# Performance work log

Measured on AMD Instinct MI355X. Metric: run time of the kernel, lower is better.

Reference implementation:

```python
import jax, jax.numpy as jnp
import numpy as np

N_NODES = 50000
N_EDGES = 1600000
D_IN = 128
D_HID = 128
D_OUT = 128


def setup_inputs() -> dict:
    key = jax.random.key(0)
    k1, k2, k3, k4, k5, k6 = jax.random.split(key, 6)
    x = jax.random.normal(k1, (N_NODES, D_IN), dtype=jnp.float32)
    edge_index = jax.random.randint(k2, (2, N_EDGES), 0, N_NODES, dtype=jnp.int64)
    # glorot-ish init for GCNConv linear weights; bias zeros-like but randomized small
    W1 = jax.random.normal(k3, (D_IN, D_HID), dtype=jnp.float32) * (1.0 / np.sqrt(D_IN))
    b1 = jax.random.normal(k4, (D_HID,), dtype=jnp.float32) * 0.01
    W2 = jax.random.normal(k5, (D_HID, D_OUT), dtype=jnp.float32) * (1.0 / np.sqrt(D_HID))
    b2 = jax.random.normal(k6, (D_OUT,), dtype=jnp.float32) * 0.01
    return {"x": x, "edge_index": edge_index, "W1": W1, "b1": b1, "W2": W2, "b2": b2}


def gcn_conv(x, src, dst, W, b, n_nodes):
    # PyG GCNConv: add self-loops, symmetric normalization deg^-1/2, lin -> aggregate -> +bias
    loop = jnp.arange(n_nodes, dtype=src.dtype)
    s = jnp.concatenate([src, loop])  # [E+N]
    d = jnp.concatenate([dst, loop])  # [E+N]
    deg = jax.ops.segment_sum(jnp.ones_like(d, dtype=x.dtype), d, num_segments=n_nodes)
    dinv = jnp.where(deg > 0, jax.lax.rsqrt(deg), 0.0)
    norm = dinv[s] * dinv[d]  # [E+N]
    h = x @ W  # [N, F_out]
    msg = h[s] * norm[:, None]  # gather + scale: [E+N, F_out]
    out = jax.ops.segment_sum(msg, d, num_segments=n_nodes)  # scatter-add
    return out + b


def reference(x, edge_index, W1, b1, W2, b2):
    src, dst = edge_index[0], edge_index[1]
    h = gcn_conv(x, src, dst, W1, b1, N_NODES)
    h = jnp.where(h >= 0, h, 0.1 * h)  # LeakyReLU(0.1)
    h = gcn_conv(h, src, dst, W2, b2, N_NODES)
    return h.mean(axis=1)  # [N]
```

## Files before the change

kernel.cpp:

```cpp
#include <hip/hip_runtime.h>
#include <hip/hip_bf16.h>


#define N_NODES 50000
#define NPAD 50048
#define D 128
#define BK 196
#define CHUNK 4096

typedef unsigned int uint;
typedef unsigned short u16;
typedef __attribute__((ext_vector_type(8))) short short8;
typedef __attribute__((ext_vector_type(4))) float floatx4;

__device__ __forceinline__ u16 cvt_bf16(float f) {
    uint u = __float_as_uint(f);
    return (u16)((u + 0x7fffu + ((u >> 16) & 1u)) >> 16);
}
__device__ __forceinline__ uint pack_bf2(float a, float b) {
    return (uint)cvt_bf16(a) | ((uint)cvt_bf16(b) << 16);
}

__global__ void hist_w2m_kernel(const int* __restrict__ dst, uint* __restrict__ H,
                                const float* __restrict__ W2, const float* __restrict__ b2,
                                float* __restrict__ w2m, uint* __restrict__ counter,
                                int E, int CHN) {
    int t = threadIdx.x, c = blockIdx.x;
    if (c < CHN) {
        __shared__ uint h[BK];
        if (t < BK) h[t] = 0;
        __syncthreads();
        int e0 = c * CHUNK;
        for (int i = t; i < CHUNK; i += 256) {
            int e = e0 + i;
            if (e < E) atomicAdd(&h[dst[e] >> 8], 1u);
        }
        __syncthreads();
        if (t < BK) H[t * CHN + c] = h[t];
    } else {
        if (t < 128) {
            float s = 0.f;
            for (int j = 0; j < 128; j++) s += W2[t * 128 + j];
            w2m[t] = s * (1.0f / 128.0f);
        } else if (t == 128) {
            float s = 0.f;
            for (int j = 0; j < 128; j++) s += b2[j];
            w2m[128] = s * (1.0f / 128.0f);
        } else if (t == 129) {
            *counter = 0;
        }
    }
}

__global__ void scan_kernel(uint* __restrict__ H, uint* __restrict__ T, uint* __restrict__ B,
                            int* __restrict__ row, uint* __restrict__ counter,
                            int CHN, int E, int N) {
    __shared__ uint s[256];
    __shared__ uint ticket_sh;
    int t = threadIdx.x, b = blockIdx.x;
    uint carry = 0;
    for (int base = 0; base < CHN; base += 256) {
        int idx = base + t;
        uint v = (idx < CHN) ? H[b * CHN + idx] : 0u;
        s[t] = v;
        __syncthreads();
#pragma unroll
        for (int off = 1; off < 256; off <<= 1) {
            uint u = (t >= off) ? s[t - off] : 0u;
            __syncthreads();
            s[t] += u;
            __syncthreads();
        }
        if (idx < CHN) H[b * CHN + idx] = carry + s[t] - v;
        carry += s[255];
        __syncthreads();
    }
    if (t == 0) {
        atomicExch(&T[b], carry);
        __threadfence();
        ticket_sh = atomicAdd(counter, 1);
    }
    __syncthreads();
    if (ticket_sh == (uint)(gridDim.x - 1)) {
        __threadfence();
        uint v = (t < BK) ? atomicAdd(&T[t], 0u) : 0u;
        s[t] = v;
        __syncthreads();
#pragma unroll
        for (int off = 1; off < 256; off <<= 1) {
            uint u = (t >= off) ? s[t - off] : 0u;
            __syncthreads();
            s[t] += u;
            __syncthreads();
        }
        if (t < BK) B[t] = s[t] - v;
        if (t == 0) { B[BK] = (uint)E; row[N] = E; }
    }
}

__global__ void scatter_kernel(const int* __restrict__ src, const int* __restrict__ dst,
                               const uint* __restrict__ H, const uint* __restrict__ B,
                               uint* __restrict__ EB, int E, int CHN) {
    __shared__ uint cur[BK];
    int t = threadIdx.x, c = blockIdx.x;
    if (t < BK) cur[t] = B[t] + H[t * CHN + c];
    __syncthreads();
    int e0 = c * CHUNK;
    for (int i = t; i < CHUNK; i += 256) {
        int e = e0 + i;
        if (e < E) {
            int d = dst[e];
            uint slot = atomicAdd(&cur[d >> 8], 1u);
            EB[slot] = ((uint)(d & 255) << 16) | (uint)src[e];
        }
    }
}

#define WT_STRIDE 136
union SortGemmSmem {
    struct { uint cnt[256], s[256], cur[256]; } sort;
    u16 wt[128 * WT_STRIDE];
};
__global__ __launch_bounds__(256) void sortgemm_kernel(
    const uint* __restrict__ EB, const uint* __restrict__ B,
    int* __restrict__ row, float* __restrict__ dinv, u16* __restrict__ esrc,
    const float* __restrict__ A, const float* __restrict__ W,
    uint* __restrict__ G32, int N, int M) {
    __shared__ SortGemmSmem sm;
    int t = threadIdx.x;

    if (blockIdx.x < BK) {
        int b = blockIdx.x;
        uint base = B[b], ne = B[b + 1] - base;
        sm.sort.cnt[t] = 0;
        __syncthreads();
        for (uint i = t; i < ne; i += 256) atomicAdd(&sm.sort.cnt[EB[base + i] >> 16], 1u);
        __syncthreads();
        uint c = sm.sort.cnt[t];
        sm.sort.s[t] = c;
        __syncthreads();
#pragma unroll
        for (int off = 1; off < 256; off <<= 1) {
            uint u = (t >= off) ? sm.sort.s[t - off] : 0u;
            __syncthreads();
            sm.sort.s[t] += u;
            __syncthreads();
        }
        uint p = sm.sort.s[t] - c;
        int v = (b << 8) + t;
        if (v < N) {
            row[v] = (int)(base + p);
            dinv[v] = rsqrtf((float)(c + 1u));
        }
        sm.sort.cur[t] = base + p;
        __syncthreads();
        for (uint i = t; i < ne; i += 256) {
            uint u = EB[base + i];
            uint slot = atomicAdd(&sm.sort.cur[u >> 16], 1u);
            esrc[slot] = (u16)(u & 0xffffu);
        }
    } else {
        int bid = blockIdx.x - BK;
        for (int i = t; i < 128 * 128; i += 256) {
            int k = i >> 7, n = i & 127;
            sm.wt[n * WT_STRIDE + k] = cvt_bf16(W[i]);
        }
        __syncthreads();

        int wave = t >> 6, lane = t & 63;
        int m = lane & 15, quad = lane >> 4;
        int rowa = bid * 64 + wave * 16 + m;
        int rowc = rowa < M ? rowa : M - 1;
        const float* Arow = A + (long)rowc * D;

        short8 afrag[4];
#pragma unroll
        for (int kt = 0; kt < 4; kt++) {
            int k0 = kt * 32 + quad * 8;
            float4 f0 = *(const float4*)(Arow + k0);
            float4 f1 = *(const float4*)(Arow + k0 + 4);
            short8 af;
            af[0] = (short)cvt_bf16(f0.x); af[1] = (short)cvt_bf16(f0.y);
            af[2] = (short)cvt_bf16(f0.z); af[3] = (short)cvt_bf16(f0.w);
            af[4] = (short)cvt_bf16(f1.x); af[5] = (short)cvt_bf16(f1.y);
            af[6] = (short)cvt_bf16(f1.z); af[7] = (short)cvt_bf16(f1.w);
            afrag[kt] = af;
        }

        int orow0 = bid * 64 + wave * 16;
        for (int n0 = 0; n0 < 128; n0 += 16) {
            floatx4 acc = {0.f, 0.f, 0.f, 0.f};
#pragma unroll
            for (int kt = 0; kt < 4; kt++) {
                short8 bf = *(const short8*)(sm.wt + (n0 + m) * WT_STRIDE + kt * 32 + quad * 8);
                acc = __builtin_amdgcn_mfma_f32_16x16x32_bf16(afrag[kt], bf, acc, 0, 0, 0);
            }
#pragma unroll
            for (int r = 0; r < 4; r++) {
                float val = acc[r];
                float oth = __shfl_xor(val, 1, 64);
                int orow = orow0 + quad * 4 + r;
                if (orow < M && (m & 1) == 0)
                    G32[(long)orow * 64 + ((n0 + m) >> 1)] = pack_bf2(val, oth);
            }
        }
    }
}

__global__ __launch_bounds__(256) void gather_node_kernel(
    const int* __restrict__ row, const u16* __restrict__ esrc,
    const uint* __restrict__ g16, const float* __restrict__ dinv,
    const float* __restrict__ b1, const float* __restrict__ w2m,
    float* __restrict__ mg, int N) {
    int wave = threadIdx.x >> 6;
    int lane = threadIdx.x & 63;
    int sub = lane & 7;
    int nb = lane >> 3;
    int v = blockIdx.x * 4 + wave;
    if (v >= N) return;

    const uint4* gv = (const uint4*)g16;
    float dvv = dinv[v];
    float acc[16];
#pragma unroll
    for (int i = 0; i < 16; i++) acc[i] = 0.f;

#define ACC8(ua, ub, wgt) {                                              \
    uint uu[8] = {(ua).x, (ua).y, (ua).z, (ua).w, (ub).x, (ub).y, (ub).z, (ub).w}; \
    _Pragma("unroll")                                                    \
    for (int i = 0; i < 8; i++) {                                        \
        acc[2*i]   += (wgt) * __uint_as_float(uu[i] << 16);              \
        acc[2*i+1] += (wgt) * __uint_as_float(uu[i] & 0xffff0000u);      \
    } }

    if (nb == 0) {
        long rb = (long)v * 16 + 2 * sub;
        uint4 ua = gv[rb], ub = gv[rb + 1];
        ACC8(ua, ub, dvv)
    }
    int jb = row[v], je = row[v + 1];
    int j = jb + nb;
    if (j < je) {
        int s0 = esrc[j];
        float wA = dinv[s0];
        long r0 = (long)s0 * 16 + 2 * sub;
        uint4 p0 = gv[r0], p1 = gv[r0 + 1];
        j += 8;
        while (j < je) {
            int s1 = esrc[j];
            float wB = dinv[s1];
            long r1 = (long)s1 * 16 + 2 * sub;
            uint4 q0 = gv[r1], q1 = gv[r1 + 1];
            j += 8;
            ACC8(p0, p1, wA)
            p0 = q0; p1 = q1; wA = wB;
        }
        ACC8(p0, p1, wA)
    }
#undef ACC8

#pragma unroll
    for (int i = 0; i < 16; i++) {
        acc[i] += __shfl_xor(acc[i], 8, 64);
        acc[i] += __shfl_xor(acc[i], 16, 64);
        acc[i] += __shfl_xor(acc[i], 32, 64);
    }

    if (nb == 0) {
        const float4* bp = (const float4*)b1;
        const float4* wp = (const float4*)w2m;
        float s = 0.f;
#pragma unroll
        for (int q4 = 0; q4 < 4; q4++) {
            float4 bb = bp[sub * 4 + q4];
            float4 wm = wp[sub * 4 + q4];
            float t0 = dvv * acc[4*q4 + 0] + bb.x; t0 = t0 >= 0.f ? t0 : 0.1f * t0;
            float t1 = dvv * acc[4*q4 + 1] + bb.y; t1 = t1 >= 0.f ? t1 : 0.1f * t1;
            float t2 = dvv * acc[4*q4 + 2] + bb.z; t2 = t2 >= 0.f ? t2 : 0.1f * t2;
            float t3 = dvv * acc[4*q4 + 3] + bb.w; t3 = t3 >= 0.f ? t3 : 0.1f * t3;
            s += t0 * wm.x + t1 * wm.y + t2 * wm.z + t3 * wm.w;
        }
        s += __shfl_xor(s, 1, 64);
        s += __shfl_xor(s, 2, 64);
        s += __shfl_xor(s, 4, 64);
        if (sub == 0) mg[v] = dvv * s;
    }
}

__global__ void out_kernel(const int* __restrict__ row, const u16* __restrict__ esrc,
                           const float* __restrict__ mg, const float* __restrict__ dinv,
                           const float* __restrict__ w2m, float* __restrict__ out, int N) {
    int v = blockIdx.x * blockDim.x + threadIdx.x;
    if (v >= N) return;
    float acc = mg[v];
    int jb = row[v], je = row[v + 1];
    int j = jb;
    for (; j + 8 <= je; j += 8) {
        acc += mg[esrc[j]] + mg[esrc[j + 1]] + mg[esrc[j + 2]] + mg[esrc[j + 3]] +
               mg[esrc[j + 4]] + mg[esrc[j + 5]] + mg[esrc[j + 6]] + mg[esrc[j + 7]];
    }
    for (; j < je; j++) acc += mg[esrc[j]];
    out[v] = dinv[v] * acc + w2m[128];
}

extern "C" void kernel_launch(void* const* d_in, const int* in_sizes, int n_in,
                              void* d_out, int out_size, void* d_ws, size_t ws_size,
                              hipStream_t stream) {
    const float* x  = (const float*)d_in[0];
    const int* ei   = (const int*)d_in[1];
    const float* W1 = (const float*)d_in[2];
    const float* b1 = (const float*)d_in[3];
    const float* W2 = (const float*)d_in[4];
    const float* b2 = (const float*)d_in[5];
    float* out = (float*)d_out;

    const int N = N_NODES;
    const int E = in_sizes[1] / 2;
    const int* src = ei;
    const int* dst = ei + E;
    const int CHN = (E + CHUNK - 1) / CHUNK;
    const int nblocks = (N + 255) / 256;

    float*    dinv    = (float*)d_ws;
    int*      row     = (int*)(dinv + NPAD);
    uint*     B       = (uint*)(row + NPAD + 16);
    float*    w2m     = (float*)(B + 256);
    float*    mg      = w2m + 256;
    uint*     T       = (uint*)(mg + NPAD);
    uint*     counter = T + 256;
    uint*     g16u    = counter + 16;
    u16*      esrc    = (u16*)(g16u + (long)NPAD * 64);
    uint*     H       = (uint*)(esrc + E);
    uint*     EB      = H + BK * CHN;

    hist_w2m_kernel<<<CHN + 1, 256, 0, stream>>>(dst, H, W2, b2, w2m, counter, E, CHN);
    scan_kernel<<<BK, 256, 0, stream>>>(H, T, B, row, counter, CHN, E, N);
    scatter_kernel<<<CHN, 256, 0, stream>>>(src, dst, H, B, EB, E, CHN);
    sortgemm_kernel<<<BK + (N + 63) / 64, 256, 0, stream>>>(EB, B, row, dinv, esrc,
                                                            x, W1, g16u, N, N);
    gather_node_kernel<<<(N + 3) / 4, 256, 0, stream>>>(row, esrc, g16u, dinv, b1, w2m, mg, N);
    out_kernel<<<nblocks, 256, 0, stream>>>(row, esrc, mg, dinv, w2m, out, N);
}
```

Before: 197.8 us.

## Fuse bucket scan into histogram via global atomics; double GEMM rows per block

Removes the separate scan kernel and the per-chunk histogram matrix. Each chunk now atomically adds its bucket counts to global totals, and the last block (chosen by ticket) computes the exclusive bucket offsets. The scatter kernel re-counts its own chunk locally and reserves space with one global atomic per bucket, so bucket placement across chunks becomes nondeterministic. The GEMM part also processes 128 rows per block instead of 64, which halves how often the weights are staged into shared memory but also halves the number of GEMM blocks. A memset is added to clear the counters.

Measured after the change: 209.3 us. 1.06x slower.

```diff
diff --git a/kernel.cpp b/kernel.cpp
--- a/kernel.cpp
+++ b/kernel.cpp
@@ -21,13 +21,17 @@
     return (uint)cvt_bf16(a) | ((uint)cvt_bf16(b) << 16);
 }
 
-__global__ void hist_w2m_kernel(const int* __restrict__ dst, uint* __restrict__ H,
+__global__ void hist_w2m_kernel(const int* __restrict__ dst,
                                 const float* __restrict__ W2, const float* __restrict__ b2,
-                                float* __restrict__ w2m, uint* __restrict__ counter,
-                                int E, int CHN) {
+                                float* __restrict__ w2m,
+                                uint* __restrict__ Tg, uint* __restrict__ counter,
+                                uint* __restrict__ B, uint* __restrict__ cur196,
+                                int* __restrict__ row, int E, int CHN, int N) {
     int t = threadIdx.x, c = blockIdx.x;
     if (c < CHN) {
         __shared__ uint h[BK];
+        __shared__ uint s[256];
+        __shared__ uint ticket_sh;
         if (t < BK) h[t] = 0;
         __syncthreads();
         int e0 = c * CHUNK;
@@ -36,81 +40,68 @@
             if (e < E) atomicAdd(&h[dst[e] >> 8], 1u);
         }
         __syncthreads();
-        if (t < BK) H[t * CHN + c] = h[t];
+        if (t < BK && h[t]) atomicAdd(&Tg[t], h[t]);
+        __syncthreads();
+        if (t == 0) {
+            __threadfence();
+            ticket_sh = atomicAdd(counter, 1);
+        }
+        __syncthreads();
+        if (ticket_sh == (uint)(CHN - 1)) {
+            __threadfence();
+            uint v = (t < BK) ? atomicAdd(&Tg[t], 0u) : 0u;
+            s[t] = v;
+            __syncthreads();
+#pragma unroll
+            for (int off = 1; off < 256; off <<= 1) {
+                uint u = (t >= off) ? s[t - off] : 0u;
+                __syncthreads();
+                s[t] += u;
+                __syncthreads();
+            }
+            if (t < BK) {
+                uint excl = s[t] - v;
+                B[t] = excl;
+                cur196[t] = excl;
+            }
+            if (t == 0) { B[BK] = (uint)E; row[N] = E; }
+        }
     } else {
         if (t < 128) {
-            float s = 0.f;
-            for (int j = 0; j < 128; j++) s += W2[t * 128 + j];
-            w2m[t] = s * (1.0f / 128.0f);
+            float sum = 0.f;
+            for (int j = 0; j < 128; j++) sum += W2[t * 128 + j];
+            w2m[t] = sum * (1.0f / 128.0f);
         } else if (t == 128) {
-            float s = 0.f;
-            for (int j = 0; j < 128; j++) s += b2[j];
-            w2m[128] = s * (1.0f / 128.0f);
-        } else if (t == 129) {
-            *counter = 0;
-        }
-    }
-}
-
-__global__ void scan_kernel(uint* __restrict__ H, uint* __restrict__ T, uint* __restrict__ B,
-                            int* __restrict__ row, uint* __restrict__ counter,
-                            int CHN, int E, int N) {
-    __shared__ uint s[256];
-    __shared__ uint ticket_sh;
-    int t = threadIdx.x, b = blockIdx.x;
-    uint carry = 0;
-    for (int base = 0; base < CHN; base += 256) {
-        int idx = base + t;
-        uint v = (idx < CHN) ? H[b * CHN + idx] : 0u;
-        s[t] = v;
-        __syncthreads();
-#pragma unroll
-        for (int off = 1; off < 256; off <<= 1) {
-            uint u = (t >= off) ? s[t - off] : 0u;
-            __syncthreads();
-            s[t] += u;
-            __syncthreads();
-        }
-        if (idx < CHN) H[b * CHN + idx] = carry + s[t] - v;
-        carry += s[255];
-        __syncthreads();
-    }
-    if (t == 0) {
-        atomicExch(&T[b], carry);
-        __threadfence();
-        ticket_sh = atomicAdd(counter, 1);
-    }
-    __syncthreads();
-    if (ticket_sh == (uint)(gridDim.x - 1)) {
-        __threadfence();
-        uint v = (t < BK) ? atomicAdd(&T[t], 0u) : 0u;
-        s[t] = v;
-        __syncthreads();
-#pragma unroll
-        for (int off = 1; off < 256; off <<= 1) {
-            uint u = (t >= off) ? s[t - off] : 0u;
-            __syncthreads();
-            s[t] += u;
-            __syncthreads();
-        }
-        if (t < BK) B[t] = s[t] - v;
-        if (t == 0) { B[BK] = (uint)E; row[N] = E; }
+            float sum = 0.f;
+            for (int j = 0; j < 128; j++) sum += b2[j];
+            w2m[128] = sum * (1.0f / 128.0f);
+        }
     }
 }
 
 __global__ void scatter_kernel(const int* __restrict__ src, const int* __restrict__ dst,
-                               const uint* __restrict__ H, const uint* __restrict__ B,
-                               uint* __restrict__ EB, int E, int CHN) {
-    __shared__ uint cur[BK];
+                               uint* __restrict__ cur196, uint* __restrict__ EB,
+                               int E, int CHN) {
+    __shared__ uint cnt[BK];
     int t = threadIdx.x, c = blockIdx.x;
-    if (t < BK) cur[t] = B[t] + H[t * CHN + c];
+    if (t < BK) cnt[t] = 0;
     __syncthreads();
     int e0 = c * CHUNK;
     for (int i = t; i < CHUNK; i += 256) {
         int e = e0 + i;
+        if (e < E) atomicAdd(&cnt[dst[e] >> 8], 1u);
+    }
+    __syncthreads();
+    if (t < BK) {
+        uint n = cnt[t];
+        cnt[t] = n ? atomicAdd(&cur196[t], n) : 0u;
+    }
+    __syncthreads();
+    for (int i = t; i < CHUNK; i += 256) {
+        int e = e0 + i;
         if (e < E) {
             int d = dst[e];
-            uint slot = atomicAdd(&cur[d >> 8], 1u);
+            uint slot = atomicAdd(&cnt[d >> 8], 1u);
             EB[slot] = ((uint)(d & 255) << 16) | (uint)src[e];
         }
     }
@@ -169,39 +160,43 @@
 
         int wave = t >> 6, lane = t & 63;
         int m = lane & 15, quad = lane >> 4;
-        int rowa = bid * 64 + wave * 16 + m;
-        int rowc = rowa < M ? rowa : M - 1;
-        const float* Arow = A + (long)rowc * D;
-
-        short8 afrag[4];
-#pragma unroll
-        for (int kt = 0; kt < 4; kt++) {
-            int k0 = kt * 32 + quad * 8;
-            float4 f0 = *(const float4*)(Arow + k0);
-            float4 f1 = *(const float4*)(Arow + k0 + 4);
-            short8 af;
-            af[0] = (short)cvt_bf16(f0.x); af[1] = (short)cvt_bf16(f0.y);
-            af[2] = (short)cvt_bf16(f0.z); af[3] = (short)cvt_bf16(f0.w);
-            af[4] = (short)cvt_bf16(f1.x); af[5] = (short)cvt_bf16(f1.y);
-            af[6] = (short)cvt_bf16(f1.z); af[7] = (short)cvt_bf16(f1.w);
-            afrag[kt] = af;
-        }
-
-        int orow0 = bid * 64 + wave * 16;
-        for (int n0 = 0; n0 < 128; n0 += 16) {
-            floatx4 acc = {0.f, 0.f, 0.f, 0.f};
+
+#pragma unroll
+        for (int rg = 0; rg < 2; rg++) {
+            int rowa = bid * 128 + rg * 64 + wave * 16 + m;
+            int rowc = rowa < M ? rowa : M - 1;
+            const float* Arow = A + (long)rowc * D;
+
+            short8 afrag[4];
 #pragma unroll
             for (int kt = 0; kt < 4; kt++) {
-                short8 bf = *(const short8*)(sm.wt + (n0 + m) * WT_STRIDE + kt * 32 + quad * 8);
-                acc = __builtin_amdgcn_mfma_f32_16x16x32_bf16(afrag[kt], bf, acc, 0, 0, 0);
+                int k0 = kt * 32 + quad * 8;
+                float4 f0 = *(const float4*)(Arow + k0);
+                float4 f1 = *(const float4*)(Arow + k0 + 4);
+                short8 af;
+                af[0] = (short)cvt_bf16(f0.x); af[1] = (short)cvt_bf16(f0.y);
+                af[2] = (short)cvt_bf16(f0.z); af[3] = (short)cvt_bf16(f0.w);
+                af[4] = (short)cvt_bf16(f1.x); af[5] = (short)cvt_bf16(f1.y);
+                af[6] = (short)cvt_bf16(f1.z); af[7] = (short)cvt_bf16(f1.w);
+                afrag[kt] = af;
             }
-#pragma unroll
-            for (int r = 0; r < 4; r++) {
-                float val = acc[r];
-                float oth = __shfl_xor(val, 1, 64);
-                int orow = orow0 + quad * 4 + r;
-                if (orow < M && (m & 1) == 0)
-                    G32[(long)orow * 64 + ((n0 + m) >> 1)] = pack_bf2(val, oth);
+
+            int orow0 = bid * 128 + rg * 64 + wave * 16;
+            for (int n0 = 0; n0 < 128; n0 += 16) {
+                floatx4 acc = {0.f, 0.f, 0.f, 0.f};
+#pragma unroll
+                for (int kt = 0; kt < 4; kt++) {
+                    short8 bf = *(const short8*)(sm.wt + (n0 + m) * WT_STRIDE + kt * 32 + quad * 8);
+                    acc = __builtin_amdgcn_mfma_f32_16x16x32_bf16(afrag[kt], bf, acc, 0, 0, 0);
+                }
+#pragma unroll
+                for (int r = 0; r < 4; r++) {
+                    float val = acc[r];
+                    float oth = __shfl_xor(val, 1, 64);
+                    int orow = orow0 + quad * 4 + r;
+                    if (orow < M && (m & 1) == 0)
+                        G32[(long)orow * 64 + ((n0 + m) >> 1)] = pack_bf2(val, oth);
+                }
             }
         }
     }
@@ -320,24 +315,27 @@
     const int* dst = ei + E;
     const int CHN = (E + CHUNK - 1) / CHUNK;
     const int nblocks = (N + 255) / 256;
+    const int GB = (N + 127) / 128;
 
     float*    dinv    = (float*)d_ws;
     int*      row     = (int*)(dinv + NPAD);
     uint*     B       = (uint*)(row + NPAD + 16);
     float*    w2m     = (float*)(B + 256);
     float*    mg      = w2m + 256;
-    uint*     T       = (uint*)(mg + NPAD);
-    uint*     counter = T + 256;
-    uint*     g16u    = counter + 16;
+    uint*     Tg      = (uint*)(mg + NPAD);
+    uint*     counter = Tg + 256;
+    uint*     cur196  = counter + 16;
+    uint*     g16u    = cur196 + 256;
     u16*      esrc    = (u16*)(g16u + (long)NPAD * 64);
-    uint*     H       = (uint*)(esrc + E);
-    uint*     EB      = H + BK * CHN;
-
-    hist_w2m_kernel<<<CHN + 1, 256, 0, stream>>>(dst, H, W2, b2, w2m, counter, E, CHN);
-    scan_kernel<<<BK, 256, 0, stream>>>(H, T, B, row, counter, CHN, E, N);
-    scatter_kernel<<<CHN, 256, 0, stream>>>(src, dst, H, B, EB, E, CHN);
-    sortgemm_kernel<<<BK + (N + 63) / 64, 256, 0, stream>>>(EB, B, row, dinv, esrc,
-                                                            x, W1, g16u, N, N);
+    uint*     EB      = (uint*)(esrc + E);
+
+    hipMemsetAsync(Tg, 0, 272 * sizeof(uint), stream);
+
+    hist_w2m_kernel<<<CHN + 1, 256, 0, stream>>>(dst, W2, b2, w2m, Tg, counter,
+                                                 B, cur196, row, E, CHN, N);
+    scatter_kernel<<<CHN, 256, 0, stream>>>(src, dst, cur196, EB, E, CHN);
+    sortgemm_kernel<<<BK + GB, 256, 0, stream>>>(EB, B, row, dinv, esrc,
+                                                 x, W1, g16u, N, N);
     gather_node_kernel<<<(N + 3) / 4, 256, 0, stream>>>(row, esrc, g16u, dinv, b1, w2m, mg, N);
     out_kernel<<<nblocks, 256, 0, stream>>>(row, esrc, mg, dinv, w2m, out, N);
 }
```
